# Kernel optimization log

Hardware: AMD Instinct MI355X
Metric: run time of the kernel (lower is better)

## Reference

```python
import jax, jax.numpy as jnp
import numpy as np

H = 1024
I = 4096
E = 8
B, S, K = 2, 2048, 2


def setup_inputs() -> dict:
    key = jax.random.key(0)
    k1, k2, k3, k4, k5, k6 = jax.random.split(key, 6)
    x = jax.random.normal(k1, (B, S, H), dtype=jnp.float32)
    expert_indices = jax.random.randint(k2, (B, S, K), 0, E, dtype=jnp.int32)
    expert_weights = jax.random.uniform(k3, (B, S, K), dtype=jnp.float32)
    gate_proj = jax.random.normal(k4, (E, I, H), dtype=jnp.float32) * 0.02
    up_proj = jax.random.normal(k5, (E, I, H), dtype=jnp.float32) * 0.02
    down_proj = jax.random.normal(k6, (E, H, I), dtype=jnp.float32) * 0.02
    return {"x": x, "expert_indices": expert_indices, "expert_weights": expert_weights,
            "gate_proj": gate_proj, "up_proj": up_proj, "down_proj": down_proj}


def reference(x, expert_indices, expert_weights, gate_proj, up_proj, down_proj):
    b, s, h = x.shape
    e = gate_proj.shape[0]
    k = expert_indices.shape[-1]
    xf = x.reshape(-1, h)                       # [N, H]
    idx = expert_indices.reshape(-1, k)         # [N, K]
    wts = expert_weights.reshape(-1, k)         # [N, K]
    # combine[n, e] = sum over slots k with idx[n,k]==e of wts[n,k]
    onehot = jax.nn.one_hot(idx, e, dtype=x.dtype)            # [N, K, E]
    combine = jnp.einsum('nk,nke->ne', wts, onehot)           # [N, E]
    out = jnp.zeros_like(xf)
    # Fixed small unrolled loop over experts (data dims fully vectorized).
    for ei in range(e):
        gate = jax.nn.silu(xf @ gate_proj[ei].T)              # [N, I]
        up = xf @ up_proj[ei].T                               # [N, I]
        out = out + ((gate * up) @ down_proj[ei].T) * combine[:, ei:ei + 1]
    return out.reshape(b, s, h)
```

## Files before the change

kernel.cpp:

```cpp
#include <hip/hip_runtime.h>
#include <hip/hip_bf16.h>
#include <cstdint>

#define HD 1024
#define ID 4096
#define NE 8
#define NTOK 4096
#define NASS 8192
#define NWL 72

typedef unsigned short u16;
typedef __attribute__((ext_vector_type(8))) __bf16 bf16x8;
typedef __attribute__((ext_vector_type(4))) float f32x4;

__device__ __forceinline__ void async16(void* lds, const void* g) {
  __builtin_amdgcn_global_load_lds(
      (const __attribute__((address_space(1))) uint32_t*)g,
      (__attribute__((address_space(3))) uint32_t*)lds, 16, 0, 0);
}

__device__ __forceinline__ u16 f2b(float f) {
  __bf16 h = (__bf16)f;
  return __builtin_bit_cast(u16, h);
}

__device__ __forceinline__ bf16x8 cvt8(const float* p) {
  const float4* q = (const float4*)p;
  float4 a = q[0], b = q[1];
  bf16x8 v;
  v[0] = (__bf16)a.x; v[1] = (__bf16)a.y; v[2] = (__bf16)a.z; v[3] = (__bf16)a.w;
  v[4] = (__bf16)b.x; v[5] = (__bf16)b.y; v[6] = (__bf16)b.z; v[7] = (__bf16)b.w;
  return v;
}

__global__ void k_pre(const float* __restrict__ x, const float* __restrict__ gate,
                      const float* __restrict__ up, u16* __restrict__ xb,
                      u16* __restrict__ wg, u16* __restrict__ wu,
                      float* __restrict__ out) {
  const size_t stride = (size_t)gridDim.x * 256;
  for (size_t v = (size_t)blockIdx.x * 256 + threadIdx.x; v < 8912896ull; v += stride) {
    const float* src; u16* dst; size_t off;
    if (v < 524288ull)        { src = x;    dst = xb; off = v;
      float4 z = {0.f, 0.f, 0.f, 0.f};
      float4* op = (float4*)(out + off * 8);
      op[0] = z; op[1] = z;
    }
    else if (v < 4718592ull)  { src = gate; dst = wg; off = v - 524288ull; }
    else                      { src = up;   dst = wu; off = v - 4718592ull; }
    size_t i8 = off * 8;
    *(bf16x8*)(dst + i8) = cvt8(src + i8);
  }
}

__global__ void k_meta(const int* __restrict__ eidx, int* __restrict__ offsets,
                       int* __restrict__ wl, int* __restrict__ tokl) {
  __shared__ int cnt[NE], offs_s[NE + 1], cur[NE];
  int t = threadIdx.x;
  if (t < NE) cnt[t] = 0;
  __syncthreads();
  for (int i = t; i < NASS; i += 1024) atomicAdd(&cnt[eidx[i]], 1);
  __syncthreads();
  if (t == 0) {
    int s = 0;
    for (int e = 0; e < NE; ++e) { offs_s[e] = s; s += cnt[e]; }
    offs_s[NE] = s;
    int w = 0;
    for (int e = 0; e < NE; ++e)
      for (int mt = 0; mt * 128 < cnt[e]; ++mt) wl[w++] = (e << 16) | mt;
    for (; w < NWL; ++w) wl[w] = -1;
  }
  if (t < NE) cur[t] = 0;
  __syncthreads();
  for (int i = t; i < NASS; i += 1024) {
    int e = eidx[i];
    int p = atomicAdd(&cur[e], 1);
    tokl[offs_s[e] + p] = i;
  }
  if (t <= NE) offsets[t] = offs_s[t];
}

__global__ __launch_bounds__(256, 2) void k_g1(
    const u16* __restrict__ xb, const u16* __restrict__ wg, const u16* __restrict__ wu,
    const float* __restrict__ down, u16* __restrict__ wd,
    const int* __restrict__ offsets, const int* __restrict__ wl,
    const int* __restrict__ tokl, u16* __restrict__ interm) {
  const int bx = blockIdx.x;
  const int t = threadIdx.x;
  if (bx >= 32) {
    int cid = (bx - 32) + 32 * (int)blockIdx.y;
    if (cid < 2048) {
#pragma unroll
      for (int l = 0; l < 8; ++l) {
        size_t i8 = (((size_t)cid * 8 + l) * 256 + t) * 8;
        *(bf16x8*)(wd + i8) = cvt8(down + i8);
      }
    }
    return;
  }
  const int wle = wl[blockIdx.y];
  if (wle < 0) return;
  const int e = wle >> 16;
  const int m0 = (wle & 0xffff) << 7;
  const int offs = offsets[e];
  const int Me = offsets[e + 1] - offs;
  const int n0 = bx * 128;
  const int lane = t & 63, wv = t >> 6;
  const int wm = wv & 1, wn = wv >> 1;

  __shared__ __align__(16) u16 As[2][128 * 32];
  __shared__ __align__(16) u16 Bg[2][128 * 32];
  __shared__ __align__(16) u16 Bu[2][128 * 32];

  const u16* asrc[2];
#pragma unroll
  for (int p = 0; p < 2; ++p) {
    int c = p * 256 + t;
    int r = c >> 2, c8 = (c & 3) * 8;
    int row = m0 + r; if (row > Me - 1) row = Me - 1;
    asrc[p] = xb + (size_t)(tokl[offs + row] >> 1) * HD + c8;
  }
  const u16 *bgsrc[2], *busrc[2];
#pragma unroll
  for (int p = 0; p < 2; ++p) {
    int c = p * 256 + t;
    int r = c >> 2, c8 = (c & 3) * 8;
    size_t boff = ((size_t)e * ID + n0 + r) * HD + c8;
    bgsrc[p] = wg + boff;
    busrc[p] = wu + boff;
  }

#define STAGE1(b, ks)                                                           \
  {                                                                             \
    _Pragma("unroll") for (int p = 0; p < 2; ++p) {                             \
      async16((char*)As[b] + (p * 256 + wv * 64) * 16, asrc[p] + (ks) * 32);    \
      async16((char*)Bg[b] + (p * 256 + wv * 64) * 16, bgsrc[p] + (ks) * 32);   \
      async16((char*)Bu[b] + (p * 256 + wv * 64) * 16, busrc[p] + (ks) * 32);   \
    }                                                                           \
  }

  f32x4 accg[4][4], accu[4][4];
#pragma unroll
  for (int mi = 0; mi < 4; ++mi)
#pragma unroll
    for (int ni = 0; ni < 4; ++ni) {
      accg[mi][ni] = (f32x4){0.f, 0.f, 0.f, 0.f};
      accu[mi][ni] = (f32x4){0.f, 0.f, 0.f, 0.f};
    }

  STAGE1(0, 0);
  __syncthreads();

  const int lrow = lane & 15, lk = (lane >> 4) * 8;
#pragma unroll 1
  for (int ks = 0; ks < HD / 32; ++ks) {
    const int curb = ks & 1;
    if (ks < HD / 32 - 1) STAGE1(curb ^ 1, ks + 1);
    bf16x8 af[4], bg[4], bu[4];
#pragma unroll
    for (int mi = 0; mi < 4; ++mi)
      af[mi] = *(const bf16x8*)&As[curb][(wm * 64 + mi * 16 + lrow) * 32 + lk];
#pragma unroll
    for (int ni = 0; ni < 4; ++ni) {
      bg[ni] = *(const bf16x8*)&Bg[curb][(wn * 64 + ni * 16 + lrow) * 32 + lk];
      bu[ni] = *(const bf16x8*)&Bu[curb][(wn * 64 + ni * 16 + lrow) * 32 + lk];
    }
#pragma unroll
    for (int mi = 0; mi < 4; ++mi)
#pragma unroll
      for (int ni = 0; ni < 4; ++ni) {
        accg[mi][ni] = __builtin_amdgcn_mfma_f32_16x16x32_bf16(af[mi], bg[ni], accg[mi][ni], 0, 0, 0);
        accu[mi][ni] = __builtin_amdgcn_mfma_f32_16x16x32_bf16(af[mi], bu[ni], accu[mi][ni], 0, 0, 0);
      }
    __syncthreads();
  }
#undef STAGE1

#pragma unroll
  for (int mi = 0; mi < 4; ++mi) {
    int rb = wm * 64 + mi * 16 + (lane >> 4) * 4;
#pragma unroll
    for (int ni = 0; ni < 4; ++ni) {
      int col = n0 + wn * 64 + ni * 16 + (lane & 15);
#pragma unroll
      for (int j = 0; j < 4; ++j) {
        int row = m0 + rb + j;
        if (row < Me) {
          float g = accg[mi][ni][j], u = accu[mi][ni][j];
          float s = g / (1.f + __expf(-g));
          interm[(size_t)(offs + row) * ID + col] = f2b(s * u);
        }
      }
    }
  }
}

__global__ __launch_bounds__(256, 2) void k_g2(
    const u16* __restrict__ interm, const u16* __restrict__ wd,
    const int* __restrict__ offsets, const int* __restrict__ wl,
    const int* __restrict__ tokl, const float* __restrict__ ewt,
    float* __restrict__ out) {
  const int wle = wl[blockIdx.y];
  if (wle < 0) return;
  const int e = wle >> 16;
  const int m0 = (wle & 0xffff) << 7;
  const int offs = offsets[e];
  const int Me = offsets[e + 1] - offs;
  const int n0 = blockIdx.x * 256;
  const int t = threadIdx.x, lane = t & 63, wv = t >> 6;
  const int wm = wv & 1, wn = wv >> 1;

  __shared__ __align__(16) u16 As[128 * 64];
  __shared__ __align__(16) u16 Bs[256 * 64];

  const u16* asrc[4];
#pragma unroll
  for (int p = 0; p < 4; ++p) {
    int c = p * 256 + t;
    int r = c >> 3, c8 = c & 7;
    int row = m0 + r; if (row > Me - 1) row = Me - 1;
    asrc[p] = interm + (size_t)(offs + row) * ID + c8 * 8;
  }
  const u16* bsrc[8];
#pragma unroll
  for (int p = 0; p < 8; ++p) {
    int c = p * 256 + t;
    int r = c >> 3, c8 = c & 7;
    bsrc[p] = wd + ((size_t)e * HD + n0 + r) * ID + c8 * 8;
  }

  f32x4 acc[4][8];
#pragma unroll
  for (int mi = 0; mi < 4; ++mi)
#pragma unroll
    for (int ni = 0; ni < 8; ++ni) acc[mi][ni] = (f32x4){0.f, 0.f, 0.f, 0.f};

  const int lrow = lane & 15, lk = (lane >> 4) * 8;
#pragma unroll 1
  for (int ks = 0; ks < ID / 64; ++ks) {
    __syncthreads();
#pragma unroll
    for (int p = 0; p < 4; ++p)
      async16((char*)As + (p * 256 + wv * 64) * 16, asrc[p]);
#pragma unroll
    for (int p = 0; p < 8; ++p)
      async16((char*)Bs + (p * 256 + wv * 64) * 16, bsrc[p]);
    __syncthreads();
#pragma unroll
    for (int kk = 0; kk < 2; ++kk) {
      bf16x8 af[4], bfr[8];
#pragma unroll
      for (int mi = 0; mi < 4; ++mi)
        af[mi] = *(const bf16x8*)&As[(wm * 64 + mi * 16 + lrow) * 64 + kk * 32 + lk];
#pragma unroll
      for (int ni = 0; ni < 8; ++ni)
        bfr[ni] = *(const bf16x8*)&Bs[(wn * 128 + ni * 16 + lrow) * 64 + kk * 32 + lk];
#pragma unroll
      for (int mi = 0; mi < 4; ++mi)
#pragma unroll
        for (int ni = 0; ni < 8; ++ni)
          acc[mi][ni] = __builtin_amdgcn_mfma_f32_16x16x32_bf16(af[mi], bfr[ni], acc[mi][ni], 0, 0, 0);
    }
#pragma unroll
    for (int p = 0; p < 4; ++p) asrc[p] += 64;
#pragma unroll
    for (int p = 0; p < 8; ++p) bsrc[p] += 64;
  }

#pragma unroll
  for (int mi = 0; mi < 4; ++mi) {
    int rb = wm * 64 + mi * 16 + (lane >> 4) * 4;
#pragma unroll
    for (int j = 0; j < 4; ++j) {
      int row = m0 + rb + j;
      if (row < Me) {
        int aid = tokl[offs + row];
        float w = ewt[aid];
        float* orow = out + (size_t)(aid >> 1) * HD;
#pragma unroll
        for (int ni = 0; ni < 8; ++ni) {
          int col = n0 + wn * 128 + ni * 16 + (lane & 15);
          atomicAdd(orow + col, w * acc[mi][ni][j]);
        }
      }
    }
  }
}

extern "C" void kernel_launch(void* const* d_in, const int* in_sizes, int n_in,
                              void* d_out, int out_size, void* d_ws, size_t ws_size,
                              hipStream_t stream) {
  const float* x    = (const float*)d_in[0];
  const int*   eidx = (const int*)d_in[1];
  const float* ewt  = (const float*)d_in[2];
  const float* gate = (const float*)d_in[3];
  const float* up   = (const float*)d_in[4];
  const float* down = (const float*)d_in[5];
  float* out = (float*)d_out;
  char* ws = (char*)d_ws;

  constexpr size_t OFF_INTERM = 0;
  constexpr size_t OFF_XB     = 67108864;
  constexpr size_t OFF_META   = 75497472;
  constexpr size_t OFF_TOK    = 75498496;
  constexpr size_t OFF_WD     = 75531264;
  constexpr size_t OFF_WG     = 142640128;
  constexpr size_t OFF_WU     = 209748992;

  u16* interm  = (u16*)(ws + OFF_INTERM);
  u16* xb      = (u16*)(ws + OFF_XB);
  int* offsets = (int*)(ws + OFF_META);
  int* wl      = (int*)(ws + OFF_META + 64);
  int* tokl    = (int*)(ws + OFF_TOK);
  u16* wd      = (u16*)(ws + OFF_WD);
  u16* wg      = (u16*)(ws + OFF_WG);
  u16* wu      = (u16*)(ws + OFF_WU);

  k_pre<<<dim3(2048), dim3(256), 0, stream>>>(x, gate, up, xb, wg, wu, out);
  k_meta<<<dim3(1), dim3(1024), 0, stream>>>(eidx, offsets, wl, tokl);
  k_g1<<<dim3(64, NWL), dim3(256), 0, stream>>>(xb, wg, wu, down, wd, offsets, wl, tokl, interm);
  k_g2<<<dim3(HD / 256, NWL), dim3(256), 0, stream>>>(interm, wd, offsets, wl, tokl, ewt, out);
}
```

Measured before the change: 460.5 us.

## Double-buffer down-proj GEMM and use partial vmcnt waits with pinned barriers

The down-projection GEMM moves from a single-buffered BK=64 loop with two block syncs per step to a double-buffered BK=32 loop. The next K-slice is prefetched with async global-to-LDS loads while MFMAs run on the current one. Both GEMMs replace __syncthreads with an explicit s_waitcnt vmcnt(6) plus a scheduling-pinned s_barrier, so only the older stage's loads are awaited. The aim is to overlap memory latency with compute. The risks are correctness if the vmcnt count does not match the six loads issued per stage, and twice as many loop iterations.

```diff
diff --git a/kernel.cpp b/kernel.cpp
--- a/kernel.cpp
+++ b/kernel.cpp
@@ -31,6 +31,12 @@
   v[0] = (__bf16)a.x; v[1] = (__bf16)a.y; v[2] = (__bf16)a.z; v[3] = (__bf16)a.w;
   v[4] = (__bf16)b.x; v[5] = (__bf16)b.y; v[6] = (__bf16)b.z; v[7] = (__bf16)b.w;
   return v;
+}
+
+__device__ __forceinline__ void pinned_barrier() {
+  __builtin_amdgcn_sched_barrier(0);
+  __builtin_amdgcn_s_barrier();
+  __builtin_amdgcn_sched_barrier(0);
 }
 
 __global__ void k_pre(const float* __restrict__ x, const float* __restrict__ gate,
@@ -148,13 +154,18 @@
     }
 
   STAGE1(0, 0);
-  __syncthreads();
 
   const int lrow = lane & 15, lk = (lane >> 4) * 8;
 #pragma unroll 1
   for (int ks = 0; ks < HD / 32; ++ks) {
     const int curb = ks & 1;
-    if (ks < HD / 32 - 1) STAGE1(curb ^ 1, ks + 1);
+    if (ks < HD / 32 - 1) {
+      STAGE1(curb ^ 1, ks + 1);
+      asm volatile("s_waitcnt vmcnt(6)" ::: "memory");
+    } else {
+      asm volatile("s_waitcnt vmcnt(0)" ::: "memory");
+    }
+    pinned_barrier();
     bf16x8 af[4], bg[4], bu[4];
 #pragma unroll
     for (int mi = 0; mi < 4; ++mi)
@@ -171,7 +182,7 @@
         accg[mi][ni] = __builtin_amdgcn_mfma_f32_16x16x32_bf16(af[mi], bg[ni], accg[mi][ni], 0, 0, 0);
         accu[mi][ni] = __builtin_amdgcn_mfma_f32_16x16x32_bf16(af[mi], bu[ni], accu[mi][ni], 0, 0, 0);
       }
-    __syncthreads();
+    pinned_barrier();
   }
 #undef STAGE1
 
@@ -209,23 +220,31 @@
   const int t = threadIdx.x, lane = t & 63, wv = t >> 6;
   const int wm = wv & 1, wn = wv >> 1;
 
-  __shared__ __align__(16) u16 As[128 * 64];
-  __shared__ __align__(16) u16 Bs[256 * 64];
-
-  const u16* asrc[4];
+  __shared__ __align__(16) u16 As[2][128 * 32];
+  __shared__ __align__(16) u16 Bs[2][256 * 32];
+
+  const u16* asrc[2];
+#pragma unroll
+  for (int p = 0; p < 2; ++p) {
+    int c = p * 256 + t;
+    int r = c >> 2, c8 = (c & 3) * 8;
+    int row = m0 + r; if (row > Me - 1) row = Me - 1;
+    asrc[p] = interm + (size_t)(offs + row) * ID + c8;
+  }
+  const u16* bsrc[4];
 #pragma unroll
   for (int p = 0; p < 4; ++p) {
     int c = p * 256 + t;
-    int r = c >> 3, c8 = c & 7;
-    int row = m0 + r; if (row > Me - 1) row = Me - 1;
-    asrc[p] = interm + (size_t)(offs + row) * ID + c8 * 8;
-  }
-  const u16* bsrc[8];
-#pragma unroll
-  for (int p = 0; p < 8; ++p) {
-    int c = p * 256 + t;
-    int r = c >> 3, c8 = c & 7;
-    bsrc[p] = wd + ((size_t)e * HD + n0 + r) * ID + c8 * 8;
+    int r = c >> 2, c8 = (c & 3) * 8;
+    bsrc[p] = wd + ((size_t)e * HD + n0 + r) * ID + c8;
+  }
+
+#define STAGE2(b, ks)                                                           \
+  {                                                                             \
+    _Pragma("unroll") for (int p = 0; p < 2; ++p)                               \
+      async16((char*)As[b] + (p * 256 + wv * 64) * 16, asrc[p] + (ks) * 32);    \
+    _Pragma("unroll") for (int p = 0; p < 4; ++p)                               \
+      async16((char*)Bs[b] + (p * 256 + wv * 64) * 16, bsrc[p] + (ks) * 32);    \
   }
 
   f32x4 acc[4][8];
@@ -233,38 +252,35 @@
   for (int mi = 0; mi < 4; ++mi)
 #pragma unroll
     for (int ni = 0; ni < 8; ++ni) acc[mi][ni] = (f32x4){0.f, 0.f, 0.f, 0.f};
+
+  STAGE2(0, 0);
 
   const int lrow = lane & 15, lk = (lane >> 4) * 8;
 #pragma unroll 1
-  for (int ks = 0; ks < ID / 64; ++ks) {
-    __syncthreads();
-#pragma unroll
-    for (int p = 0; p < 4; ++p)
-      async16((char*)As + (p * 256 + wv * 64) * 16, asrc[p]);
-#pragma unroll
-    for (int p = 0; p < 8; ++p)
-      async16((char*)Bs + (p * 256 + wv * 64) * 16, bsrc[p]);
-    __syncthreads();
-#pragma unroll
-    for (int kk = 0; kk < 2; ++kk) {
-      bf16x8 af[4], bfr[8];
-#pragma unroll
-      for (int mi = 0; mi < 4; ++mi)
-        af[mi] = *(const bf16x8*)&As[(wm * 64 + mi * 16 + lrow) * 64 + kk * 32 + lk];
+  for (int ks = 0; ks < ID / 32; ++ks) {
+    const int curb = ks & 1;
+    if (ks < ID / 32 - 1) {
+      STAGE2(curb ^ 1, ks + 1);
+      asm volatile("s_waitcnt vmcnt(6)" ::: "memory");
+    } else {
+      asm volatile("s_waitcnt vmcnt(0)" ::: "memory");
+    }
+    pinned_barrier();
+    bf16x8 af[4], bfr[8];
+#pragma unroll
+    for (int mi = 0; mi < 4; ++mi)
+      af[mi] = *(const bf16x8*)&As[curb][(wm * 64 + mi * 16 + lrow) * 32 + lk];
+#pragma unroll
+    for (int ni = 0; ni < 8; ++ni)
+      bfr[ni] = *(const bf16x8*)&Bs[curb][(wn * 128 + ni * 16 + lrow) * 32 + lk];
+#pragma unroll
+    for (int mi = 0; mi < 4; ++mi)
 #pragma unroll
       for (int ni = 0; ni < 8; ++ni)
-        bfr[ni] = *(const bf16x8*)&Bs[(wn * 128 + ni * 16 + lrow) * 64 + kk * 32 + lk];
-#pragma unroll
-      for (int mi = 0; mi < 4; ++mi)
-#pragma unroll
-        for (int ni = 0; ni < 8; ++ni)
-          acc[mi][ni] = __builtin_amdgcn_mfma_f32_16x16x32_bf16(af[mi], bfr[ni], acc[mi][ni], 0, 0, 0);
-    }
-#pragma unroll
-    for (int p = 0; p < 4; ++p) asrc[p] += 64;
-#pragma unroll
-    for (int p = 0; p < 8; ++p) bsrc[p] += 64;
-  }
+        acc[mi][ni] = __builtin_amdgcn_mfma_f32_16x16x32_bf16(af[mi], bfr[ni], acc[mi][ni], 0, 0, 0);
+    pinned_barrier();
+  }
+#undef STAGE2
 
 #pragma unroll
   for (int mi = 0; mi < 4; ++mi) {
```

Result: no change. 463.9 us, median of 2 (+0.7%).
